# Optimization experiments

Hardware: AMD Instinct MI355X
Metric: run time of the kernel (lower is better)

Reference implementation:

```python
import jax, jax.numpy as jnp
import numpy as np

COMMITMENT_COST = 0.25
ENTROPY_LOSS_RATIO = 0.1
ENTROPY_TEMPERATURE = 0.01


def squared_euclidean_distance(a, b):
    # a: [N, D], b: [K, D] -> [N, K]
    a2 = jnp.sum(a * a, axis=1, keepdims=True)          # [N, 1]
    b2 = jnp.sum(b * b, axis=1)[None, :]                # [1, K]
    ab = jnp.matmul(a, b.T)                             # [N, K]
    return a2 - 2.0 * ab + b2


def entropy_loss(affinity, temperature):
    # MaskGIT-style softmax entropy loss; affinity: [..., K]
    flat = affinity.reshape(-1, affinity.shape[-1]) / temperature
    probs = jax.nn.softmax(flat, axis=-1)
    log_probs = jax.nn.log_softmax(flat + 1e-5, axis=-1)
    target_probs = probs
    avg_probs = jnp.mean(target_probs, axis=0)
    avg_entropy = -jnp.sum(avg_probs * jnp.log(avg_probs + 1e-5))
    sample_entropy = -jnp.mean(jnp.sum(target_probs * log_probs, axis=-1))
    return sample_entropy - avg_entropy


def reference(x, codebook):
    # x: [B, H, W, D], codebook: [K, D]
    K = codebook.shape[0]
    flat_x = x.reshape(-1, x.shape[-1])
    distances = squared_euclidean_distance(flat_x, codebook).reshape(x.shape[:-1] + (K,))
    encoding_indices = jnp.argmin(distances, axis=-1)        # [B, H, W]
    encodings = jax.nn.one_hot(encoding_indices, K, dtype=x.dtype)
    quantized = jnp.dot(encodings, codebook)                 # [B, H, W, D]

    e_latent_loss = jnp.mean((jax.lax.stop_gradient(quantized) - x) ** 2) * COMMITMENT_COST
    q_latent_loss = jnp.mean((quantized - jax.lax.stop_gradient(x)) ** 2)
    ent_loss = entropy_loss(-distances, ENTROPY_TEMPERATURE) * ENTROPY_LOSS_RATIO
    loss = (e_latent_loss + q_latent_loss + ent_loss).astype(jnp.float32)

    # straight-through estimator
    quantized = x + jax.lax.stop_gradient(quantized - x)
    return quantized, loss, encoding_indices


def setup_inputs() -> dict:
    key = jax.random.key(0)
    k1, k2 = jax.random.split(key)
    x = jax.random.normal(k1, (128, 16, 16, 256), dtype=jnp.float32)
    codebook = jax.random.normal(k2, (1024, 256), dtype=jnp.float32)
    return {"x": x, "codebook": codebook}
```

## Files before the change

### kernel.cpp

```cpp
#include <hip/hip_runtime.h>
#include <math.h>

typedef unsigned short u16;
typedef unsigned int u32;
typedef unsigned long long u64;
typedef float    f32x4  __attribute__((ext_vector_type(4)));
typedef __bf16   bf16x8 __attribute__((ext_vector_type(8)));

#define NS    32768
#define KC    1024
#define INV_T 100.0f
#define TAU   2.0f

#define C2_OFF   0
#define SUMM_OFF 1024
#define SUMM_SZ  (NS * 32 * 2)
#define HIST_OFF (SUMM_OFF + SUMM_SZ)
#define PD_OFF   (HIST_OFF + KC)
#define PS_OFF   (PD_OFF + 8192)

#define XTILE_U16 8192
#define CTILE_U16 8192

__device__ __forceinline__ u16 f2bf(float f) {
    unsigned u = __float_as_uint(f);
    return (u16)((u + 0x7FFFu + ((u >> 16) & 1u)) >> 16);
}

__device__ __forceinline__ void gload_lds16(const void* g, void* l) {
    __builtin_amdgcn_global_load_lds((const __attribute__((address_space(1))) void*)g,
                                     (__attribute__((address_space(3))) void*)l, 16, 0, 0);
}

__global__ __launch_bounds__(256) void vq_xcvt(const float* __restrict__ x,
                                               u16* __restrict__ xb) {
    const int tl = blockIdx.x;
    const int t = threadIdx.x;
    const float* src = x + (size_t)tl * 32 * 256;
    u16* dst = xb + (size_t)tl * XTILE_U16;
    #pragma unroll
    for (int j = 0; j < 4; ++j) {
        int row = j * 8 + (t >> 5);
        int kq0 = (t & 31) * 2;
        #pragma unroll
        for (int h = 0; h < 2; ++h) {
            int kq = kq0 + h;
            float4 v = reinterpret_cast<const float4*>(src)[(size_t)row * 64 + kq];
            int kk = kq * 4;
            int kss = kk >> 5;
            int sub = (kk >> 3) & 3;
            int half = kq & 1;
            ushort4 o;
            o.x = f2bf(v.x); o.y = f2bf(v.y); o.z = f2bf(v.z); o.w = f2bf(v.w);
            *reinterpret_cast<ushort4*>(
                dst + ((size_t)kss * 128 + sub * 32 + row) * 8 + half * 4) = o;
        }
    }
}

__global__ __launch_bounds__(256) void vq_cbprep(const float* __restrict__ cb,
                                                 u16* __restrict__ ct,
                                                 float* __restrict__ c2,
                                                 float* __restrict__ hist) {
    const int b = blockIdx.x;
    const int t = threadIdx.x, w = t >> 6, lane = t & 63;

    if (t < 16) hist[b * 16 + t] = 0.f;

    #pragma unroll
    for (int i = 0; i < 4; ++i) {
        int g = b * 16 + i * 4 + w;
        float4 v = reinterpret_cast<const float4*>(cb)[(size_t)g * 64 + lane];
        float s = v.x * v.x + v.y * v.y + v.z * v.z + v.w * v.w;
        #pragma unroll
        for (int off = 32; off; off >>= 1) s += __shfl_xor(s, off);
        if (lane == 0) c2[g] = s;
    }

    const int T = b >> 1, p = b & 1;
    #pragma unroll
    for (int i = 0; i < 2; ++i) {
        int c = p * 512 + i * 256 + t;
        int ks = c >> 7, sub = (c >> 5) & 3, row = c & 31;
        const float* srcp = cb + (size_t)(T * 32 + row) * 256 + ks * 32 + sub * 8;
        float4 a0 = *reinterpret_cast<const float4*>(srcp);
        float4 a1 = *reinterpret_cast<const float4*>(srcp + 4);
        bf16x8 v;
        v[0]=(__bf16)a0.x; v[1]=(__bf16)a0.y; v[2]=(__bf16)a0.z; v[3]=(__bf16)a0.w;
        v[4]=(__bf16)a1.x; v[5]=(__bf16)a1.y; v[6]=(__bf16)a1.z; v[7]=(__bf16)a1.w;
        *reinterpret_cast<bf16x8*>(ct + (size_t)T * CTILE_U16 + (size_t)c * 8) = v;
    }
}

__global__ __launch_bounds__(256, 4) void vq_dist(const u16* __restrict__ xb,
                                                  const u16* __restrict__ ct,
                                                  const float* __restrict__ c2,
                                                  float2* __restrict__ summ) {
    __shared__ __align__(16) u16 Bs[2][CTILE_U16];

    const int id = blockIdx.x;
    const int xcd = id & 7, j = id >> 3;
    const int sq = xcd * 32 + (j >> 2);
    const int q  = j & 3;
    const int sBase = sq * 128;

    const int t = threadIdx.x, w = t >> 6, lane = t & 63;
    const int lo16 = lane & 15, hi = lane >> 4;
    const int hi4 = hi * 4;

    #define STAGE(buf, bt)                                                        \
        do {                                                                      \
            const u16* bT_ = ct + (size_t)(bt) * CTILE_U16;                       \
            _Pragma("unroll")                                                     \
            for (int i_ = 0; i_ < 4; ++i_) {                                      \
                int c0_ = (i_ * 4 + w) * 64;                                      \
                gload_lds16(bT_ + (size_t)(c0_ + lane) * 8, &Bs[buf][c0_ * 8]);   \
            }                                                                     \
        } while (0)

    STAGE(0, q * 8);

    const u16* aT = xb + (size_t)(sq * 4 + w) * XTILE_U16;
    bf16x8 af[2][8];
    #pragma unroll
    for (int sm = 0; sm < 2; ++sm)
        #pragma unroll
        for (int ks = 0; ks < 8; ++ks)
            af[sm][ks] = *reinterpret_cast<const bf16x8*>(
                aT + ((size_t)ks * 128 + hi * 32 + sm * 16 + lo16) * 8);
    __syncthreads();

    int cur = 0;
    for (int tt = 0; tt < 8; ++tt) {
        if (tt < 7) STAGE(cur ^ 1, q * 8 + tt + 1);

        f32x4 acc[2][2];
        #pragma unroll
        for (int cn = 0; cn < 2; ++cn)
            #pragma unroll
            for (int sm = 0; sm < 2; ++sm) acc[cn][sm] = (f32x4)0.f;

        const u16* bsc = &Bs[cur][0];
        #pragma unroll
        for (int ks = 0; ks < 8; ++ks) {
            bf16x8 bfr[2];
            #pragma unroll
            for (int cn = 0; cn < 2; ++cn)
                bfr[cn] = *reinterpret_cast<const bf16x8*>(
                    &bsc[((size_t)ks * 128 + hi * 32 + cn * 16 + lo16) * 8]);
            #pragma unroll
            for (int cn = 0; cn < 2; ++cn)
                #pragma unroll
                for (int sm = 0; sm < 2; ++sm)
                    acc[cn][sm] = __builtin_amdgcn_mfma_f32_16x16x32_bf16(
                        bfr[cn], af[sm][ks], acc[cn][sm], 0, 0, 0);
        }

        const int cBase = q * 256 + tt * 32;
        float c2v[2][4];
        #pragma unroll
        for (int cn = 0; cn < 2; ++cn)
            #pragma unroll
            for (int r = 0; r < 4; ++r)
                c2v[cn][r] = c2[cBase + cn * 16 + hi4 + r];

        #pragma unroll
        for (int sm = 0; sm < 2; ++sm) {
            float dd[2][4];
            #pragma unroll
            for (int cn = 0; cn < 2; ++cn)
                #pragma unroll
                for (int r = 0; r < 4; ++r)
                    dd[cn][r] = fmaf(-2.0f, acc[cn][sm][r], c2v[cn][r]);
            float bm = dd[0][0];
            #pragma unroll
            for (int cn = 0; cn < 2; ++cn)
                #pragma unroll
                for (int r = 0; r < 4; ++r) bm = fminf(bm, dd[cn][r]);
            bm = fminf(bm, __shfl_xor(bm, 16));
            bm = fminf(bm, __shfl_xor(bm, 32));
            const float thr = bm + TAU;
            u32 m32 = 0;
            #pragma unroll
            for (int cn = 0; cn < 2; ++cn)
                #pragma unroll
                for (int r = 0; r < 4; ++r)
                    m32 |= (dd[cn][r] < thr ? 1u : 0u) << (cn * 16 + hi4 + r);
            m32 |= __shfl_xor(m32, 16);
            m32 |= __shfl_xor(m32, 32);
            if (hi == 0) {
                const int R = sBase + w * 32 + sm * 16 + lo16;
                float2 o; o.x = bm; o.y = __uint_as_float(m32);
                summ[(size_t)R * 32 + q * 8 + tt] = o;
            }
        }
        __syncthreads();
        cur ^= 1;
    }
    #undef STAGE
}

__global__ __launch_bounds__(256) void vq_refine(const float* __restrict__ x,
                                                 const float* __restrict__ cb,
                                                 const float* __restrict__ c2,
                                                 const float2* __restrict__ summ,
                                                 float* __restrict__ hist,
                                                 float* __restrict__ pd,
                                                 float* __restrict__ ps,
                                                 float* __restrict__ outq,
                                                 float* __restrict__ out_idx_f) {
    __shared__ int   cd_k[4][128];
    __shared__ float cd_d[4][128];
    __shared__ float rd[4], rs[4];

    const int wid = threadIdx.x >> 6, lane = threadIdx.x & 63;
    const int s = blockIdx.x * 4 + wid;
    const float4 xv = reinterpret_cast<const float4*>(x)[(size_t)s * 64 + lane];

    float x2s = xv.x * xv.x + xv.y * xv.y + xv.z * xv.z + xv.w * xv.w;
    #pragma unroll
    for (int off = 32; off; off >>= 1) x2s += __shfl_xor(x2s, off);

    const float2 smv = summ[(size_t)s * 32 + (lane & 31)];
    float gm = smv.x;
    #pragma unroll
    for (int off = 1; off < 32; off <<= 1) gm = fminf(gm, __shfl_xor(gm, off));
    const float lim = gm + TAU;

    u64 act = __ballot((lane < 32) && (smv.x <= lim));

    const float4* cb4 = reinterpret_cast<const float4*>(cb);
    float m = 3.4e38f, S1 = 0.f, S2 = 0.f;
    int bk = 0, cnt = 0;

    while (act) {
        const int hb = __ffsll(act) - 1; act &= act - 1;
        u32 mk = __float_as_uint(__shfl(smv.y, hb));
        while (mk) {
            int vc = 1;
            int b0 = __ffs(mk) - 1; mk &= mk - 1;
            int k0 = hb * 32 + b0, k1 = k0, k2 = k0, k3 = k0;
            if (mk) { int b = __ffs(mk) - 1; mk &= mk - 1; k1 = hb * 32 + b; vc = 2; }
            if (mk) { int b = __ffs(mk) - 1; mk &= mk - 1; k2 = hb * 32 + b; vc = 3; }
            if (mk) { int b = __ffs(mk) - 1; mk &= mk - 1; k3 = hb * 32 + b; vc = 4; }

            float4 cv0 = cb4[(size_t)k0 * 64 + lane];
            float4 cv1 = cb4[(size_t)k1 * 64 + lane];
            float4 cv2 = cb4[(size_t)k2 * 64 + lane];
            float4 cv3 = cb4[(size_t)k3 * 64 + lane];
            float r0 = xv.x*cv0.x + xv.y*cv0.y + xv.z*cv0.z + xv.w*cv0.w;
            float r1 = xv.x*cv1.x + xv.y*cv1.y + xv.z*cv1.z + xv.w*cv1.w;
            float r2 = xv.x*cv2.x + xv.y*cv2.y + xv.z*cv2.z + xv.w*cv2.w;
            float r3 = xv.x*cv3.x + xv.y*cv3.y + xv.z*cv3.z + xv.w*cv3.w;
            #pragma unroll
            for (int off = 32; off; off >>= 1) {
                r0 += __shfl_xor(r0, off);
                r1 += __shfl_xor(r1, off);
                r2 += __shfl_xor(r2, off);
                r3 += __shfl_xor(r3, off);
            }
            float dk[4];
            dk[0] = (x2s - 2.0f * r0) + c2[k0];
            dk[1] = (x2s - 2.0f * r1) + c2[k1];
            dk[2] = (x2s - 2.0f * r2) + c2[k2];
            dk[3] = (x2s - 2.0f * r3) + c2[k3];
            int kk[4] = {k0, k1, k2, k3};

            #pragma unroll
            for (int jj = 0; jj < 4; ++jj) {
                if (jj >= vc) break;
                float d = dk[jj];
                if (lane == 0 && cnt < 128) { cd_k[wid][cnt] = kk[jj]; cd_d[wid][cnt] = d; }
                ++cnt;
                if (S1 == 0.f)   { m = d; S1 = 1.f; S2 = 0.f; bk = kk[jj]; }
                else if (d < m)  { float f = __expf((d - m) * INV_T);
                                   S2 = f * (S2 + (m - d) * S1);
                                   S1 = S1 * f + 1.f; m = d; bk = kk[jj]; }
                else             { float e = __expf((m - d) * INV_T);
                                   S1 += e; S2 += e * (d - m); }
            }
        }
    }
    float sent = S2 * INV_T / S1 + logf(S1);
    if (lane == 0) { rd[wid] = m; rs[wid] = sent; }
    __syncthreads();

    if (cnt > 128) cnt = 128;
    for (int c = lane; c < cnt; c += 64) {
        float dkv = cd_d[wid][c]; int k = cd_k[wid][c];
        atomicAdd(&hist[k], __expf((m - dkv) * INV_T) / S1);
    }

    reinterpret_cast<float4*>(outq)[(size_t)s * 64 + lane] = cb4[(size_t)bk * 64 + lane];
    if (lane == 0) out_idx_f[s] = (float)bk;

    if (threadIdx.x == 0) {
        pd[blockIdx.x] = rd[0] + rd[1] + rd[2] + rd[3];
        ps[blockIdx.x] = rs[0] + rs[1] + rs[2] + rs[3];
    }
}

__global__ __launch_bounds__(256) void vq_finalize(const float* __restrict__ hist,
                                                   const float* __restrict__ pd,
                                                   const float* __restrict__ ps,
                                                   float* __restrict__ loss_out) {
    float ae = 0.f, sd = 0.f, se = 0.f;
    for (int k = threadIdx.x; k < KC; k += 256) {
        float p = hist[k] * (1.0f / (float)NS);
        ae += -p * logf(p + 1e-5f);
    }
    for (int b = threadIdx.x; b < 8192; b += 256) { sd += pd[b]; se += ps[b]; }
    #pragma unroll
    for (int off = 32; off; off >>= 1) {
        ae += __shfl_xor(ae, off); sd += __shfl_xor(sd, off); se += __shfl_xor(se, off);
    }
    __shared__ float r[3][4];
    int wid = threadIdx.x >> 6, lane = threadIdx.x & 63;
    if (lane == 0) { r[0][wid] = ae; r[1][wid] = sd; r[2][wid] = se; }
    __syncthreads();
    if (threadIdx.x == 0) {
        float AE = r[0][0] + r[0][1] + r[0][2] + r[0][3];
        float SD = r[1][0] + r[1][1] + r[1][2] + r[1][3];
        float SE = r[2][0] + r[2][1] + r[2][2] + r[2][3];
        float latent = 1.25f * SD / 8388608.0f;
        loss_out[0] = latent + 0.1f * (SE * (1.0f / (float)NS) - AE);
    }
}

extern "C" void kernel_launch(void* const* d_in, const int* in_sizes, int n_in,
                              void* d_out, int out_size, void* d_ws, size_t ws_size,
                              hipStream_t stream) {
    const float* x  = (const float*)d_in[0];
    const float* cb = (const float*)d_in[1];
    float* out = (float*)d_out;
    float* ws  = (float*)d_ws;

    u16* xb = (u16*)d_out;
    u16* ct = (u16*)(out + 4194304);

    vq_xcvt<<<1024, 256, 0, stream>>>(x, xb);
    vq_cbprep<<<64, 256, 0, stream>>>(cb, ct, ws + C2_OFF, ws + HIST_OFF);
    vq_dist<<<1024, 256, 0, stream>>>(xb, ct, ws + C2_OFF, (float2*)(ws + SUMM_OFF));
    vq_refine<<<NS / 4, 256, 0, stream>>>(x, cb, ws + C2_OFF,
                                          (const float2*)(ws + SUMM_OFF),
                                          ws + HIST_OFF, ws + PD_OFF, ws + PS_OFF,
                                          out, out + 8388609);
    vq_finalize<<<1, 256, 0, stream>>>(ws + HIST_OFF, ws + PD_OFF, ws + PS_OFF,
                                       out + 8388608);
}
```

Before: 88.58 us.

## Process two samples per wavefront in refine, precompute x norms, tighten candidate threshold

The refine kernel now assigns each 32-lane half-wave to its own sample, so every wave handles two rows and the grid shrinks by half. Row squared norms are computed during the bf16 conversion kernel and read back instead of being reduced again in refine. The candidate threshold TAU drops from 2.0 to 1.25, so fewer codebook entries are recomputed exactly in fp32. The tighter threshold risks dropping near-tie candidates that the bf16 approximation mis-ranks, and it also leaves fewer terms in the entropy histogram.

```diff
diff --git a/kernel.cpp b/kernel.cpp
--- a/kernel.cpp
+++ b/kernel.cpp
@@ -10,14 +10,15 @@
 #define NS    32768
 #define KC    1024
 #define INV_T 100.0f
-#define TAU   2.0f
+#define TAU   1.25f
 
 #define C2_OFF   0
-#define SUMM_OFF 1024
+#define X2_OFF   1024
+#define SUMM_OFF (1024 + 32768)
 #define SUMM_SZ  (NS * 32 * 2)
 #define HIST_OFF (SUMM_OFF + SUMM_SZ)
 #define PD_OFF   (HIST_OFF + KC)
-#define PS_OFF   (PD_OFF + 8192)
+#define PS_OFF   (PD_OFF + 4096)
 
 #define XTILE_U16 8192
 #define CTILE_U16 8192
@@ -33,7 +34,8 @@
 }
 
 __global__ __launch_bounds__(256) void vq_xcvt(const float* __restrict__ x,
-                                               u16* __restrict__ xb) {
+                                               u16* __restrict__ xb,
+                                               float* __restrict__ x2) {
     const int tl = blockIdx.x;
     const int t = threadIdx.x;
     const float* src = x + (size_t)tl * 32 * 256;
@@ -42,10 +44,12 @@
     for (int j = 0; j < 4; ++j) {
         int row = j * 8 + (t >> 5);
         int kq0 = (t & 31) * 2;
+        float sq = 0.f;
         #pragma unroll
         for (int h = 0; h < 2; ++h) {
             int kq = kq0 + h;
             float4 v = reinterpret_cast<const float4*>(src)[(size_t)row * 64 + kq];
+            sq += v.x * v.x + v.y * v.y + v.z * v.z + v.w * v.w;
             int kk = kq * 4;
             int kss = kk >> 5;
             int sub = (kk >> 3) & 3;
@@ -55,6 +59,10 @@
             *reinterpret_cast<ushort4*>(
                 dst + ((size_t)kss * 128 + sub * 32 + row) * 8 + half * 4) = o;
         }
+        sq += __shfl_xor(sq, 1);  sq += __shfl_xor(sq, 2);
+        sq += __shfl_xor(sq, 4);  sq += __shfl_xor(sq, 8);
+        sq += __shfl_xor(sq, 16);
+        if ((t & 31) == 0) x2[tl * 32 + row] = sq;
     }
 }
 
@@ -203,39 +211,44 @@
 __global__ __launch_bounds__(256) void vq_refine(const float* __restrict__ x,
                                                  const float* __restrict__ cb,
                                                  const float* __restrict__ c2,
+                                                 const float* __restrict__ x2,
                                                  const float2* __restrict__ summ,
                                                  float* __restrict__ hist,
                                                  float* __restrict__ pd,
                                                  float* __restrict__ ps,
                                                  float* __restrict__ outq,
                                                  float* __restrict__ out_idx_f) {
-    __shared__ int   cd_k[4][128];
-    __shared__ float cd_d[4][128];
-    __shared__ float rd[4], rs[4];
+    __shared__ int   cd_k[4][2][64];
+    __shared__ float cd_d[4][2][64];
+    __shared__ float rd[8], rs[8];
 
     const int wid = threadIdx.x >> 6, lane = threadIdx.x & 63;
-    const int s = blockIdx.x * 4 + wid;
-    const float4 xv = reinterpret_cast<const float4*>(x)[(size_t)s * 64 + lane];
-
-    float x2s = xv.x * xv.x + xv.y * xv.y + xv.z * xv.z + xv.w * xv.w;
-    #pragma unroll
-    for (int off = 32; off; off >>= 1) x2s += __shfl_xor(x2s, off);
-
-    const float2 smv = summ[(size_t)s * 32 + (lane & 31)];
+    const int half = lane >> 5, l32 = lane & 31;
+    const int s = blockIdx.x * 8 + wid * 2 + half;
+
+    const float4* x4  = reinterpret_cast<const float4*>(x);
+    const float4* cb4 = reinterpret_cast<const float4*>(cb);
+
+    const float4 xr0 = x4[(size_t)s * 64 + l32];
+    const float4 xr1 = x4[(size_t)s * 64 + 32 + l32];
+    const float x2s = x2[s];
+
+    const float2 smv = summ[(size_t)s * 32 + l32];
     float gm = smv.x;
-    #pragma unroll
-    for (int off = 1; off < 32; off <<= 1) gm = fminf(gm, __shfl_xor(gm, off));
+    gm = fminf(gm, __shfl_xor(gm, 1));  gm = fminf(gm, __shfl_xor(gm, 2));
+    gm = fminf(gm, __shfl_xor(gm, 4));  gm = fminf(gm, __shfl_xor(gm, 8));
+    gm = fminf(gm, __shfl_xor(gm, 16));
     const float lim = gm + TAU;
 
-    u64 act = __ballot((lane < 32) && (smv.x <= lim));
-
-    const float4* cb4 = reinterpret_cast<const float4*>(cb);
+    u64 ball = __ballot(smv.x <= lim);
+    u32 act = (u32)(ball >> (half * 32));
+
     float m = 3.4e38f, S1 = 0.f, S2 = 0.f;
     int bk = 0, cnt = 0;
 
     while (act) {
-        const int hb = __ffsll(act) - 1; act &= act - 1;
-        u32 mk = __float_as_uint(__shfl(smv.y, hb));
+        const int hb = __ffs(act) - 1; act &= act - 1;
+        u32 mk = __float_as_uint(__shfl(smv.y, half * 32 + hb));
         while (mk) {
             int vc = 1;
             int b0 = __ffs(mk) - 1; mk &= mk - 1;
@@ -244,16 +257,20 @@
             if (mk) { int b = __ffs(mk) - 1; mk &= mk - 1; k2 = hb * 32 + b; vc = 3; }
             if (mk) { int b = __ffs(mk) - 1; mk &= mk - 1; k3 = hb * 32 + b; vc = 4; }
 
-            float4 cv0 = cb4[(size_t)k0 * 64 + lane];
-            float4 cv1 = cb4[(size_t)k1 * 64 + lane];
-            float4 cv2 = cb4[(size_t)k2 * 64 + lane];
-            float4 cv3 = cb4[(size_t)k3 * 64 + lane];
-            float r0 = xv.x*cv0.x + xv.y*cv0.y + xv.z*cv0.z + xv.w*cv0.w;
-            float r1 = xv.x*cv1.x + xv.y*cv1.y + xv.z*cv1.z + xv.w*cv1.w;
-            float r2 = xv.x*cv2.x + xv.y*cv2.y + xv.z*cv2.z + xv.w*cv2.w;
-            float r3 = xv.x*cv3.x + xv.y*cv3.y + xv.z*cv3.z + xv.w*cv3.w;
-            #pragma unroll
-            for (int off = 32; off; off >>= 1) {
+            float4 a0 = cb4[(size_t)k0 * 64 + l32], b0v = cb4[(size_t)k0 * 64 + 32 + l32];
+            float4 a1 = cb4[(size_t)k1 * 64 + l32], b1v = cb4[(size_t)k1 * 64 + 32 + l32];
+            float4 a2 = cb4[(size_t)k2 * 64 + l32], b2v = cb4[(size_t)k2 * 64 + 32 + l32];
+            float4 a3 = cb4[(size_t)k3 * 64 + l32], b3v = cb4[(size_t)k3 * 64 + 32 + l32];
+            float r0 = xr0.x*a0.x + xr0.y*a0.y + xr0.z*a0.z + xr0.w*a0.w
+                     + xr1.x*b0v.x + xr1.y*b0v.y + xr1.z*b0v.z + xr1.w*b0v.w;
+            float r1 = xr0.x*a1.x + xr0.y*a1.y + xr0.z*a1.z + xr0.w*a1.w
+                     + xr1.x*b1v.x + xr1.y*b1v.y + xr1.z*b1v.z + xr1.w*b1v.w;
+            float r2 = xr0.x*a2.x + xr0.y*a2.y + xr0.z*a2.z + xr0.w*a2.w
+                     + xr1.x*b2v.x + xr1.y*b2v.y + xr1.z*b2v.z + xr1.w*b2v.w;
+            float r3 = xr0.x*a3.x + xr0.y*a3.y + xr0.z*a3.z + xr0.w*a3.w
+                     + xr1.x*b3v.x + xr1.y*b3v.y + xr1.z*b3v.z + xr1.w*b3v.w;
+            #pragma unroll
+            for (int off = 1; off < 32; off <<= 1) {
                 r0 += __shfl_xor(r0, off);
                 r1 += __shfl_xor(r1, off);
                 r2 += __shfl_xor(r2, off);
@@ -270,7 +287,7 @@
             for (int jj = 0; jj < 4; ++jj) {
                 if (jj >= vc) break;
                 float d = dk[jj];
-                if (lane == 0 && cnt < 128) { cd_k[wid][cnt] = kk[jj]; cd_d[wid][cnt] = d; }
+                if (l32 == 0 && cnt < 64) { cd_k[wid][half][cnt] = kk[jj]; cd_d[wid][half][cnt] = d; }
                 ++cnt;
                 if (S1 == 0.f)   { m = d; S1 = 1.f; S2 = 0.f; bk = kk[jj]; }
                 else if (d < m)  { float f = __expf((d - m) * INV_T);
@@ -282,21 +299,25 @@
         }
     }
     float sent = S2 * INV_T / S1 + logf(S1);
-    if (lane == 0) { rd[wid] = m; rs[wid] = sent; }
+    if (l32 == 0) { rd[wid * 2 + half] = m; rs[wid * 2 + half] = sent; }
+
+    if (cnt > 64) cnt = 64;
+    for (int c = l32; c < cnt; c += 32) {
+        float dkv = cd_d[wid][half][c]; int k = cd_k[wid][half][c];
+        atomicAdd(&hist[k], __expf((m - dkv) * INV_T) / S1);
+    }
+
+    reinterpret_cast<float4*>(outq)[(size_t)s * 64 + l32]      = cb4[(size_t)bk * 64 + l32];
+    reinterpret_cast<float4*>(outq)[(size_t)s * 64 + 32 + l32] = cb4[(size_t)bk * 64 + 32 + l32];
+    if (l32 == 0) out_idx_f[s] = (float)bk;
+
     __syncthreads();
-
-    if (cnt > 128) cnt = 128;
-    for (int c = lane; c < cnt; c += 64) {
-        float dkv = cd_d[wid][c]; int k = cd_k[wid][c];
-        atomicAdd(&hist[k], __expf((m - dkv) * INV_T) / S1);
-    }
-
-    reinterpret_cast<float4*>(outq)[(size_t)s * 64 + lane] = cb4[(size_t)bk * 64 + lane];
-    if (lane == 0) out_idx_f[s] = (float)bk;
-
     if (threadIdx.x == 0) {
-        pd[blockIdx.x] = rd[0] + rd[1] + rd[2] + rd[3];
-        ps[blockIdx.x] = rs[0] + rs[1] + rs[2] + rs[3];
+        float sd = 0.f, se = 0.f;
+        #pragma unroll
+        for (int i = 0; i < 8; ++i) { sd += rd[i]; se += rs[i]; }
+        pd[blockIdx.x] = sd;
+        ps[blockIdx.x] = se;
     }
 }
 
@@ -309,7 +330,7 @@
         float p = hist[k] * (1.0f / (float)NS);
         ae += -p * logf(p + 1e-5f);
     }
-    for (int b = threadIdx.x; b < 8192; b += 256) { sd += pd[b]; se += ps[b]; }
+    for (int b = threadIdx.x; b < 4096; b += 256) { sd += pd[b]; se += ps[b]; }
     #pragma unroll
     for (int off = 32; off; off >>= 1) {
         ae += __shfl_xor(ae, off); sd += __shfl_xor(sd, off); se += __shfl_xor(se, off);
@@ -338,10 +359,10 @@
     u16* xb = (u16*)d_out;
     u16* ct = (u16*)(out + 4194304);
 
-    vq_xcvt<<<1024, 256, 0, stream>>>(x, xb);
+    vq_xcvt<<<1024, 256, 0, stream>>>(x, xb, ws + X2_OFF);
     vq_cbprep<<<64, 256, 0, stream>>>(cb, ct, ws + C2_OFF, ws + HIST_OFF);
     vq_dist<<<1024, 256, 0, stream>>>(xb, ct, ws + C2_OFF, (float2*)(ws + SUMM_OFF));
-    vq_refine<<<NS / 4, 256, 0, stream>>>(x, cb, ws + C2_OFF,
+    vq_refine<<<NS / 8, 256, 0, stream>>>(x, cb, ws + C2_OFF, ws + X2_OFF,
                                           (const float2*)(ws + SUMM_OFF),
                                           ws + HIST_OFF, ws + PD_OFF, ws + PS_OFF,
                                           out, out + 8388609);
```

New measurement: 80.86 us. -8.7%, faster.
